# Performance work log

Measured on AMD Instinct MI355X. Metric: run time of the kernel, lower is better.

Reference implementation:

```python
import jax, jax.numpy as jnp
import numpy as np

N_NODES = 1_000_000   # nodal points, 3 DOFs each
N_ELEMS = 500_000     # H8 (8-node hexahedral) elements
N_TYPES = 64          # distinct element stiffness matrices (24x24)


def setup_inputs() -> dict:
    key = jax.random.key(0)
    k1, k2, k3, k4 = jax.random.split(key, 4)
    U = jax.random.normal(k1, (N_NODES, 3), dtype=jnp.float32)
    filters = jax.random.normal(k2, (N_TYPES, 24, 24), dtype=jnp.float32)
    H8types = jax.random.randint(k3, (N_ELEMS,), 0, N_TYPES, dtype=jnp.int32)
    nodIdx = jax.random.randint(k4, (N_ELEMS, 8), 0, N_NODES, dtype=jnp.int32)
    return {"U": U, "filters": filters, "H8types": H8types, "nodIdx": nodIdx}


def reference(U, filters, H8types, nodIdx):
    """FEM stiffness matvec KU = sum_e scatter(K_type(e) @ gather(U, e)).

    U:       [N, 3]      nodal displacements (3 DOFs per node)
    filters: [T, 24, 24] per-type element stiffness matrices
    H8types: [E]         element type index into filters
    nodIdx:  [E, 8]      element -> node connectivity
    returns KU: [N, 3]
    """
    E = nodIdx.shape[0]
    # gather the 8 nodes x 3 DOFs of each element -> [E, 24]
    ue = U[nodIdx].reshape(E, 24)
    # per-type stiffness for each element -> [E, 24, 24]
    Ke = filters[H8types]
    # per-element force vector f_e = K_e @ u_e -> [E, 24]
    fe = jnp.einsum('eij,ej->ei', Ke, ue)
    # scatter-add element forces back to nodal DOFs
    KU = jnp.zeros_like(U).at[nodIdx.reshape(-1)].add(fe.reshape(E * 8, 3))
    return KU
```

## Files before the change

kernel.cpp:

```cpp
#include <hip/hip_runtime.h>


#define NTYPES    64
#define KSTRIDE   580
#define RSHIFT    11
#define RNODES    2048
#define MAXB      512
#define CAP       10240
#define K1_TPB    1024
#define K1_EPT    2
#define K1_CHUNK  (K1_TPB * K1_EPT)
#define K2_TPB    1024
#define PREP_TPB  256

typedef int          nint4  __attribute__((ext_vector_type(4)));
typedef unsigned int nuint2 __attribute__((ext_vector_type(2)));
typedef unsigned int nuint4 __attribute__((ext_vector_type(4)));

__device__ __forceinline__ unsigned bf16_rne(float f) {
    unsigned b = __float_as_uint(f);
    return (b + 0x7FFFu + ((b >> 16) & 1u)) >> 16;
}


__global__ __launch_bounds__(PREP_TPB) void pack_u_kernel(
    const float* __restrict__ U, nuint2* __restrict__ Ub,
    float* __restrict__ KU, unsigned* __restrict__ tails,
    int n_nodes, int n_buckets)
{
    int n = blockIdx.x * PREP_TPB + threadIdx.x;
    if (n < n_buckets) tails[n] = 0;
    if (n >= n_nodes) return;
    const float* up = U + (size_t)n * 3;
    unsigned bx = bf16_rne(up[0]);
    unsigned by = bf16_rne(up[1]);
    unsigned bz = bf16_rne(up[2]);
    nuint2 v = { bx | (by << 16), bz };
    Ub[n] = v;
    KU[3 * n + 0] = 0.f;
    KU[3 * n + 1] = 0.f;
    KU[3 * n + 2] = 0.f;
}


__global__ __launch_bounds__(K1_TPB, 4) void feconv_bin_kernel(
    const nuint2* __restrict__ Ub,
    const float* __restrict__ K,
    const int*   __restrict__ types,
    const int*   __restrict__ nodIdx,
    float*       __restrict__ KU,
    unsigned*    __restrict__ tails,
    nuint2*      __restrict__ recs,
    int n_elems, int n_buckets)
{
    extern __shared__ float sK[];
    __shared__ unsigned       sCnt[MAXB];
    __shared__ unsigned       sBase[MAXB];
    __shared__ unsigned       sTCnt[NTYPES];
    __shared__ unsigned       sTOff[NTYPES];
    __shared__ unsigned short sOrder[K1_CHUNK];
    __shared__ unsigned char  sType[K1_CHUNK];

    for (int w = threadIdx.x; w < NTYPES * 576; w += K1_TPB) {
        int t = w / 576;
        int r = w - t * 576;
        sK[t * KSTRIDE + r] = K[w];
    }
    for (int i = threadIdx.x; i < n_buckets; i += K1_TPB) sCnt[i] = 0;
    if (threadIdx.x < NTYPES) sTCnt[threadIdx.x] = 0;
    __syncthreads();

    const int base = blockIdx.x * K1_CHUNK;
    int cnt_chunk = n_elems - base;
    if (cnt_chunk > K1_CHUNK) cnt_chunk = K1_CHUNK;

    int myT[K1_EPT];
#pragma unroll
    for (int k = 0; k < K1_EPT; ++k) {
        int li = threadIdx.x + k * K1_TPB;
        myT[k] = -1;
        if (li < cnt_chunk) {
            int t = __builtin_nontemporal_load(&types[base + li]);
            myT[k] = t;
            sType[li] = (unsigned char)t;
            atomicAdd(&sTCnt[t], 1u);
        }
    }
    __syncthreads();

    if (threadIdx.x < NTYPES) {
        unsigned v = sTCnt[threadIdx.x];
        unsigned s = v;
#pragma unroll
        for (int d = 1; d < NTYPES; d <<= 1) {
            unsigned o = __shfl_up(s, d, 64);
            if ((int)threadIdx.x >= d) s += o;
        }
        sTOff[threadIdx.x] = s - v;
        sTCnt[threadIdx.x] = 0;
    }
    __syncthreads();

#pragma unroll
    for (int k = 0; k < K1_EPT; ++k) {
        int li = threadIdx.x + k * K1_TPB;
        if (myT[k] >= 0) {
            unsigned p = sTOff[myT[k]] + atomicAdd(&sTCnt[myT[k]], 1u);
            sOrder[p] = (unsigned short)li;
        }
    }
    __syncthreads();

    int     nodes[K1_EPT][8];
    int     tt[K1_EPT];
    nuint2  uu[K1_EPT][8];

#pragma unroll
    for (int k = 0; k < K1_EPT; ++k) {
        int slot = threadIdx.x + k * K1_TPB;
        tt[k] = -1;
        if (slot < cnt_chunk) {
            int li = sOrder[slot];
            int e  = base + li;
            tt[k] = sType[li];
            const nint4* q = (const nint4*)(nodIdx + (size_t)e * 8);
            nint4 a = q[0];
            nint4 b = q[1];
            nodes[k][0] = a.x; nodes[k][1] = a.y; nodes[k][2] = a.z; nodes[k][3] = a.w;
            nodes[k][4] = b.x; nodes[k][5] = b.y; nodes[k][6] = b.z; nodes[k][7] = b.w;
#pragma unroll
            for (int j = 0; j < 8; ++j)
                uu[k][j] = Ub[nodes[k][j]];
#pragma unroll
            for (int j = 0; j < 8; ++j)
                atomicAdd(&sCnt[(unsigned)nodes[k][j] >> RSHIFT], 1u);
        }
    }
    __syncthreads();

    for (int b = threadIdx.x; b < n_buckets; b += K1_TPB) {
        unsigned c = sCnt[b];
        sBase[b] = c ? atomicAdd(&tails[b], c) : 0u;
        sCnt[b] = 0;
    }
    __syncthreads();

#pragma unroll
    for (int k = 0; k < K1_EPT; ++k) {
        if (tt[k] < 0) continue;

        float ue[24];
#pragma unroll
        for (int j = 0; j < 8; ++j) {
            nuint2 v = uu[k][j];
            ue[3 * j + 0] = __uint_as_float(v.x << 16);
            ue[3 * j + 1] = __uint_as_float(v.x & 0xFFFF0000u);
            ue[3 * j + 2] = __uint_as_float(v.y << 16);
        }

        const float4* Kt4 = (const float4*)(sK + tt[k] * KSTRIDE);
#pragma unroll
        for (int j = 0; j < 8; ++j) {
            float a0 = 0.f, a1 = 0.f, a2 = 0.f;
#pragma unroll
            for (int q = 0; q < 6; ++q) {
                float4 k0 = Kt4[(3 * j + 0) * 6 + q];
                float4 k1 = Kt4[(3 * j + 1) * 6 + q];
                float4 k2 = Kt4[(3 * j + 2) * 6 + q];
                float u0 = ue[4 * q + 0], u1 = ue[4 * q + 1];
                float u2 = ue[4 * q + 2], u3 = ue[4 * q + 3];
                a0 += k0.x * u0 + k0.y * u1 + k0.z * u2 + k0.w * u3;
                a1 += k1.x * u0 + k1.y * u1 + k1.z * u2 + k1.w * u3;
                a2 += k2.x * u0 + k2.y * u1 + k2.z * u2 + k2.w * u3;
            }
            unsigned n = (unsigned)nodes[k][j];
            unsigned b = n >> RSHIFT;
            unsigned pos = sBase[b] + atomicAdd(&sCnt[b], 1u);
            if (pos < CAP) {
                unsigned local = n & (RNODES - 1);
                nuint2 r = { bf16_rne(a0) | (bf16_rne(a1) << 16),
                             bf16_rne(a2) | (local << 16) };
                recs[(size_t)b * CAP + pos] = r;
            } else {
                atomicAdd(&KU[(size_t)n * 3 + 0], a0);
                atomicAdd(&KU[(size_t)n * 3 + 1], a1);
                atomicAdd(&KU[(size_t)n * 3 + 2], a2);
            }
        }
    }
}


__global__ __launch_bounds__(K2_TPB) void feconv_acc_kernel(
    const nuint2*   __restrict__ recs,
    const unsigned* __restrict__ tails,
    float*          __restrict__ KU,
    int n_nodes)
{
    __shared__ float sAcc[RNODES * 3];
    const int b = blockIdx.x;

    for (int i = threadIdx.x; i < RNODES * 3; i += K2_TPB) sAcc[i] = 0.f;
    __syncthreads();

    unsigned cnt = tails[b];
    if (cnt > CAP) cnt = CAP;
    const nuint2* base = recs + (size_t)b * CAP;
    const nuint4* base4 = (const nuint4*)base;

    unsigned npairs = cnt >> 1;
    for (unsigned i = threadIdx.x; i < npairs; i += K2_TPB) {
        nuint4 p = base4[i];
        unsigned o0 = (p.y >> 16) * 3;
        atomicAdd(&sAcc[o0 + 0], __uint_as_float(p.x << 16));
        atomicAdd(&sAcc[o0 + 1], __uint_as_float(p.x & 0xFFFF0000u));
        atomicAdd(&sAcc[o0 + 2], __uint_as_float(p.y << 16));
        unsigned o1 = (p.w >> 16) * 3;
        atomicAdd(&sAcc[o1 + 0], __uint_as_float(p.z << 16));
        atomicAdd(&sAcc[o1 + 1], __uint_as_float(p.z & 0xFFFF0000u));
        atomicAdd(&sAcc[o1 + 2], __uint_as_float(p.w << 16));
    }
    if ((cnt & 1u) && threadIdx.x == 0) {
        nuint2 r = base[cnt - 1];
        unsigned o = (r.y >> 16) * 3;
        atomicAdd(&sAcc[o + 0], __uint_as_float(r.x << 16));
        atomicAdd(&sAcc[o + 1], __uint_as_float(r.x & 0xFFFF0000u));
        atomicAdd(&sAcc[o + 2], __uint_as_float(r.y << 16));
    }
    __syncthreads();

    const int nbase = b * RNODES;
    int limit = n_nodes - nbase;
    if (limit > RNODES) limit = RNODES;
    limit *= 3;
    float* out = KU + (size_t)nbase * 3;
    for (int i = threadIdx.x; i < limit; i += K2_TPB) out[i] += sAcc[i];
}


__global__ __launch_bounds__(256) void feconv_elem_kernel(
    const float* __restrict__ U, const float* __restrict__ K,
    const int* __restrict__ types, const int* __restrict__ nodIdx,
    float* __restrict__ KU, int n_elems)
{
    int e = blockIdx.x * blockDim.x + threadIdx.x;
    if (e >= n_elems) return;
    int t = types[e];
    const int4* idx4 = (const int4*)(nodIdx + (size_t)e * 8);
    int4 iA = idx4[0], iB = idx4[1];
    int nodes[8] = {iA.x, iA.y, iA.z, iA.w, iB.x, iB.y, iB.z, iB.w};
    float ue[24];
#pragma unroll
    for (int j = 0; j < 8; ++j) {
        const float* up = U + (size_t)nodes[j] * 3;
        ue[3 * j + 0] = up[0]; ue[3 * j + 1] = up[1]; ue[3 * j + 2] = up[2];
    }
    const float* Kt = K + (size_t)t * 576;
#pragma unroll
    for (int i = 0; i < 24; ++i) {
        const float4* row = (const float4*)(Kt + i * 24);
        float acc = 0.f;
#pragma unroll
        for (int q = 0; q < 6; ++q) {
            float4 k = row[q];
            acc += k.x * ue[4 * q + 0] + k.y * ue[4 * q + 1]
                 + k.z * ue[4 * q + 2] + k.w * ue[4 * q + 3];
        }
        atomicAdd(&KU[(size_t)nodes[i / 3] * 3 + (i % 3)], acc);
    }
}

extern "C" void kernel_launch(void* const* d_in, const int* in_sizes, int n_in,
                              void* d_out, int out_size, void* d_ws, size_t ws_size,
                              hipStream_t stream) {
    const float* U      = (const float*)d_in[0];
    const float* Kf     = (const float*)d_in[1];
    const int*   types  = (const int*)d_in[2];
    const int*   nodIdx = (const int*)d_in[3];
    float*       KU     = (float*)d_out;

    const int n_elems = in_sizes[2];
    const int n_nodes = in_sizes[0] / 3;
    const int n_buckets = (n_nodes + RNODES - 1) / RNODES;

    const size_t ub_off  = 4096;
    const size_t rec_off = ub_off + (((size_t)n_nodes * 8 + 255) & ~255ull);
    const size_t need    = rec_off + (size_t)n_buckets * CAP * 8;

    if (n_buckets <= MAXB && ws_size >= need) {
        unsigned* tails = (unsigned*)d_ws;
        nuint2*   Ub    = (nuint2*)((char*)d_ws + ub_off);
        nuint2*   recs  = (nuint2*)((char*)d_ws + rec_off);

        int gridP = (n_nodes + PREP_TPB - 1) / PREP_TPB;
        pack_u_kernel<<<gridP, PREP_TPB, 0, stream>>>(
            U, Ub, KU, tails, n_nodes, n_buckets);

        size_t lds_bytes = (size_t)NTYPES * KSTRIDE * sizeof(float);
        int grid1 = (n_elems + K1_CHUNK - 1) / K1_CHUNK;
        feconv_bin_kernel<<<grid1, K1_TPB, lds_bytes, stream>>>(
            Ub, Kf, types, nodIdx, KU, tails, recs, n_elems, n_buckets);
        feconv_acc_kernel<<<n_buckets, K2_TPB, 0, stream>>>(
            recs, tails, KU, n_nodes);
    } else {
        (void)hipMemsetAsync(KU, 0, (size_t)out_size * sizeof(float), stream);
        int block = 256;
        int grid = (n_elems + block - 1) / block;
        feconv_elem_kernel<<<grid, block, 0, stream>>>(
            U, Kf, types, nodIdx, KU, n_elems);
    }
}
```

Before: 214.2 us.

## Read stiffness matrices from global memory instead of staging in LDS

Removes the per-block copy of all 64 stiffness matrices (about 148 KB) into shared memory, so the binning kernel reads K directly from global memory through the caches. Because elements are sorted by type within each block, neighbouring threads tend to read the same K rows. The block shrinks to 512 threads with one element per thread and higher occupancy hints, which also removes the per-block staging cost. In exchange, every multiply-accumulate now loads K from the L1/L2 caches instead of LDS, and each block has fewer elements to amortise its binning overhead.

Result: slower. 256.5 us (+19.8%).

```diff
diff --git a/kernel.cpp b/kernel.cpp
--- a/kernel.cpp
+++ b/kernel.cpp
@@ -2,13 +2,12 @@
 
 
 #define NTYPES    64
-#define KSTRIDE   580
 #define RSHIFT    11
 #define RNODES    2048
 #define MAXB      512
 #define CAP       10240
-#define K1_TPB    1024
-#define K1_EPT    2
+#define K1_TPB    512
+#define K1_EPT    1
 #define K1_CHUNK  (K1_TPB * K1_EPT)
 #define K2_TPB    1024
 #define PREP_TPB  256
@@ -43,7 +42,7 @@
 }
 
 
-__global__ __launch_bounds__(K1_TPB, 4) void feconv_bin_kernel(
+__global__ __launch_bounds__(K1_TPB, 6) void feconv_bin_kernel(
     const nuint2* __restrict__ Ub,
     const float* __restrict__ K,
     const int*   __restrict__ types,
@@ -53,7 +52,6 @@
     nuint2*      __restrict__ recs,
     int n_elems, int n_buckets)
 {
-    extern __shared__ float sK[];
     __shared__ unsigned       sCnt[MAXB];
     __shared__ unsigned       sBase[MAXB];
     __shared__ unsigned       sTCnt[NTYPES];
@@ -61,11 +59,6 @@
     __shared__ unsigned short sOrder[K1_CHUNK];
     __shared__ unsigned char  sType[K1_CHUNK];
 
-    for (int w = threadIdx.x; w < NTYPES * 576; w += K1_TPB) {
-        int t = w / 576;
-        int r = w - t * 576;
-        sK[t * KSTRIDE + r] = K[w];
-    }
     for (int i = threadIdx.x; i < n_buckets; i += K1_TPB) sCnt[i] = 0;
     if (threadIdx.x < NTYPES) sTCnt[threadIdx.x] = 0;
     __syncthreads();
@@ -74,14 +67,12 @@
     int cnt_chunk = n_elems - base;
     if (cnt_chunk > K1_CHUNK) cnt_chunk = K1_CHUNK;
 
-    int myT[K1_EPT];
-#pragma unroll
-    for (int k = 0; k < K1_EPT; ++k) {
-        int li = threadIdx.x + k * K1_TPB;
-        myT[k] = -1;
+    int myT = -1;
+    {
+        int li = threadIdx.x;
         if (li < cnt_chunk) {
             int t = __builtin_nontemporal_load(&types[base + li]);
-            myT[k] = t;
+            myT = t;
             sType[li] = (unsigned char)t;
             atomicAdd(&sTCnt[t], 1u);
         }
@@ -101,40 +92,31 @@
     }
     __syncthreads();
 
-#pragma unroll
-    for (int k = 0; k < K1_EPT; ++k) {
-        int li = threadIdx.x + k * K1_TPB;
-        if (myT[k] >= 0) {
-            unsigned p = sTOff[myT[k]] + atomicAdd(&sTCnt[myT[k]], 1u);
-            sOrder[p] = (unsigned short)li;
-        }
-    }
-    __syncthreads();
-
-    int     nodes[K1_EPT][8];
-    int     tt[K1_EPT];
-    nuint2  uu[K1_EPT][8];
-
-#pragma unroll
-    for (int k = 0; k < K1_EPT; ++k) {
-        int slot = threadIdx.x + k * K1_TPB;
-        tt[k] = -1;
-        if (slot < cnt_chunk) {
-            int li = sOrder[slot];
-            int e  = base + li;
-            tt[k] = sType[li];
-            const nint4* q = (const nint4*)(nodIdx + (size_t)e * 8);
-            nint4 a = q[0];
-            nint4 b = q[1];
-            nodes[k][0] = a.x; nodes[k][1] = a.y; nodes[k][2] = a.z; nodes[k][3] = a.w;
-            nodes[k][4] = b.x; nodes[k][5] = b.y; nodes[k][6] = b.z; nodes[k][7] = b.w;
-#pragma unroll
-            for (int j = 0; j < 8; ++j)
-                uu[k][j] = Ub[nodes[k][j]];
-#pragma unroll
-            for (int j = 0; j < 8; ++j)
-                atomicAdd(&sCnt[(unsigned)nodes[k][j] >> RSHIFT], 1u);
-        }
+    if (myT >= 0) {
+        unsigned p = sTOff[myT] + atomicAdd(&sTCnt[myT], 1u);
+        sOrder[p] = (unsigned short)threadIdx.x;
+    }
+    __syncthreads();
+
+    int    tt = -1;
+    int    nodes[8];
+    nuint2 uu[8];
+
+    if (threadIdx.x < cnt_chunk) {
+        int li = sOrder[threadIdx.x];
+        int e  = base + li;
+        tt = sType[li];
+        const nint4* q = (const nint4*)(nodIdx + (size_t)e * 8);
+        nint4 a = q[0];
+        nint4 b = q[1];
+        nodes[0] = a.x; nodes[1] = a.y; nodes[2] = a.z; nodes[3] = a.w;
+        nodes[4] = b.x; nodes[5] = b.y; nodes[6] = b.z; nodes[7] = b.w;
+#pragma unroll
+        for (int j = 0; j < 8; ++j)
+            uu[j] = Ub[nodes[j]];
+#pragma unroll
+        for (int j = 0; j < 8; ++j)
+            atomicAdd(&sCnt[(unsigned)nodes[j] >> RSHIFT], 1u);
     }
     __syncthreads();
 
@@ -145,20 +127,17 @@
     }
     __syncthreads();
 
-#pragma unroll
-    for (int k = 0; k < K1_EPT; ++k) {
-        if (tt[k] < 0) continue;
-
+    if (tt >= 0) {
         float ue[24];
 #pragma unroll
         for (int j = 0; j < 8; ++j) {
-            nuint2 v = uu[k][j];
+            nuint2 v = uu[j];
             ue[3 * j + 0] = __uint_as_float(v.x << 16);
             ue[3 * j + 1] = __uint_as_float(v.x & 0xFFFF0000u);
             ue[3 * j + 2] = __uint_as_float(v.y << 16);
         }
 
-        const float4* Kt4 = (const float4*)(sK + tt[k] * KSTRIDE);
+        const float4* Kt4 = (const float4*)(K + (size_t)tt * 576);
 #pragma unroll
         for (int j = 0; j < 8; ++j) {
             float a0 = 0.f, a1 = 0.f, a2 = 0.f;
@@ -173,7 +152,7 @@
                 a1 += k1.x * u0 + k1.y * u1 + k1.z * u2 + k1.w * u3;
                 a2 += k2.x * u0 + k2.y * u1 + k2.z * u2 + k2.w * u3;
             }
-            unsigned n = (unsigned)nodes[k][j];
+            unsigned n = (unsigned)nodes[j];
             unsigned b = n >> RSHIFT;
             unsigned pos = sBase[b] + atomicAdd(&sCnt[b], 1u);
             if (pos < CAP) {
@@ -296,9 +275,8 @@
         pack_u_kernel<<<gridP, PREP_TPB, 0, stream>>>(
             U, Ub, KU, tails, n_nodes, n_buckets);
 
-        size_t lds_bytes = (size_t)NTYPES * KSTRIDE * sizeof(float);
         int grid1 = (n_elems + K1_CHUNK - 1) / K1_CHUNK;
-        feconv_bin_kernel<<<grid1, K1_TPB, lds_bytes, stream>>>(
+        feconv_bin_kernel<<<grid1, K1_TPB, 0, stream>>>(
             Ub, Kf, types, nodIdx, KU, tails, recs, n_elems, n_buckets);
         feconv_acc_kernel<<<n_buckets, K2_TPB, 0, stream>>>(
             recs, tails, KU, n_nodes);
```

## Split element type range across block pairs to halve LDS stiffness footprint

Applied to the files above, without the earlier changes.

Each element window is now handled by two blocks, each loading only half of the stiffness-matrix types into LDS and processing the elements whose type falls in its half. This halves per-block LDS so more blocks can reside per CU (launch bounds raised), at the cost of doubling the K preload and the type reads per window, and leaving half-empty thread slots. Bucket granularity is also coarsened (larger node ranges, larger capacity), and KSTRIDE padding is removed, which may introduce LDS bank conflicts.

Result: slower. 274.3 us (+28.1%).

```diff
diff --git a/kernel.cpp b/kernel.cpp
--- a/kernel.cpp
+++ b/kernel.cpp
@@ -2,14 +2,14 @@
 
 
 #define NTYPES    64
-#define KSTRIDE   580
-#define RSHIFT    11
-#define RNODES    2048
-#define MAXB      512
-#define CAP       10240
+#define HTYPES    32
+#define KWORDS    576
+#define RSHIFT    12
+#define RNODES    4096
+#define MAXB      256
+#define CAP       20480
 #define K1_TPB    1024
-#define K1_EPT    2
-#define K1_CHUNK  (K1_TPB * K1_EPT)
+#define WCHUNK    2048
 #define K2_TPB    1024
 #define PREP_TPB  256
 
@@ -43,7 +43,7 @@
 }
 
 
-__global__ __launch_bounds__(K1_TPB, 4) void feconv_bin_kernel(
+__global__ __launch_bounds__(K1_TPB, 8) void feconv_bin_kernel(
     const nuint2* __restrict__ Ub,
     const float* __restrict__ K,
     const int*   __restrict__ types,
@@ -56,44 +56,43 @@
     extern __shared__ float sK[];
     __shared__ unsigned       sCnt[MAXB];
     __shared__ unsigned       sBase[MAXB];
-    __shared__ unsigned       sTCnt[NTYPES];
-    __shared__ unsigned       sTOff[NTYPES];
-    __shared__ unsigned short sOrder[K1_CHUNK];
-    __shared__ unsigned char  sType[K1_CHUNK];
-
-    for (int w = threadIdx.x; w < NTYPES * 576; w += K1_TPB) {
-        int t = w / 576;
-        int r = w - t * 576;
-        sK[t * KSTRIDE + r] = K[w];
-    }
+    __shared__ unsigned       sTCnt[HTYPES];
+    __shared__ unsigned       sTOff[HTYPES];
+    __shared__ unsigned short sOrder[WCHUNK];
+
+    const int window = blockIdx.x >> 1;
+    const int typeLo = (blockIdx.x & 1) * HTYPES;
+    const int base   = window * WCHUNK;
+    int cnt_chunk = n_elems - base;
+    if (cnt_chunk > WCHUNK) cnt_chunk = WCHUNK;
+
+    for (int w = threadIdx.x; w < HTYPES * KWORDS; w += K1_TPB)
+        sK[w] = K[(size_t)typeLo * KWORDS + w];
     for (int i = threadIdx.x; i < n_buckets; i += K1_TPB) sCnt[i] = 0;
-    if (threadIdx.x < NTYPES) sTCnt[threadIdx.x] = 0;
-    __syncthreads();
-
-    const int base = blockIdx.x * K1_CHUNK;
-    int cnt_chunk = n_elems - base;
-    if (cnt_chunk > K1_CHUNK) cnt_chunk = K1_CHUNK;
-
-    int myT[K1_EPT];
-#pragma unroll
-    for (int k = 0; k < K1_EPT; ++k) {
+    if (threadIdx.x < HTYPES) sTCnt[threadIdx.x] = 0;
+    __syncthreads();
+
+    int myT[2];
+#pragma unroll
+    for (int k = 0; k < 2; ++k) {
         int li = threadIdx.x + k * K1_TPB;
         myT[k] = -1;
         if (li < cnt_chunk) {
-            int t = __builtin_nontemporal_load(&types[base + li]);
-            myT[k] = t;
-            sType[li] = (unsigned char)t;
-            atomicAdd(&sTCnt[t], 1u);
-        }
-    }
-    __syncthreads();
-
-    if (threadIdx.x < NTYPES) {
+            int rel = __builtin_nontemporal_load(&types[base + li]) - typeLo;
+            if ((unsigned)rel < HTYPES) {
+                myT[k] = rel;
+                atomicAdd(&sTCnt[rel], 1u);
+            }
+        }
+    }
+    __syncthreads();
+
+    if (threadIdx.x < HTYPES) {
         unsigned v = sTCnt[threadIdx.x];
         unsigned s = v;
 #pragma unroll
-        for (int d = 1; d < NTYPES; d <<= 1) {
-            unsigned o = __shfl_up(s, d, 64);
+        for (int d = 1; d < HTYPES; d <<= 1) {
+            unsigned o = __shfl_up(s, d, HTYPES);
             if ((int)threadIdx.x >= d) s += o;
         }
         sTOff[threadIdx.x] = s - v;
@@ -102,27 +101,30 @@
     __syncthreads();
 
 #pragma unroll
-    for (int k = 0; k < K1_EPT; ++k) {
-        int li = threadIdx.x + k * K1_TPB;
+    for (int k = 0; k < 2; ++k) {
         if (myT[k] >= 0) {
+            int li = threadIdx.x + k * K1_TPB;
             unsigned p = sTOff[myT[k]] + atomicAdd(&sTCnt[myT[k]], 1u);
-            sOrder[p] = (unsigned short)li;
-        }
-    }
-    __syncthreads();
-
-    int     nodes[K1_EPT][8];
-    int     tt[K1_EPT];
-    nuint2  uu[K1_EPT][8];
-
-#pragma unroll
-    for (int k = 0; k < K1_EPT; ++k) {
+            sOrder[p] = (unsigned short)(li | (myT[k] << 11));
+        }
+    }
+    __syncthreads();
+
+    const int cntHalf = (int)(sTOff[HTYPES - 1] + sTCnt[HTYPES - 1]);
+
+    int    tt[2];
+    int    nodes[2][8];
+    nuint2 uu[2][8];
+
+#pragma unroll
+    for (int k = 0; k < 2; ++k) {
         int slot = threadIdx.x + k * K1_TPB;
         tt[k] = -1;
-        if (slot < cnt_chunk) {
-            int li = sOrder[slot];
-            int e  = base + li;
-            tt[k] = sType[li];
+        if (slot < cntHalf) {
+            unsigned od = sOrder[slot];
+            int li  = od & (WCHUNK - 1);
+            tt[k]   = od >> 11;
+            int e   = base + li;
             const nint4* q = (const nint4*)(nodIdx + (size_t)e * 8);
             nint4 a = q[0];
             nint4 b = q[1];
@@ -146,7 +148,7 @@
     __syncthreads();
 
 #pragma unroll
-    for (int k = 0; k < K1_EPT; ++k) {
+    for (int k = 0; k < 2; ++k) {
         if (tt[k] < 0) continue;
 
         float ue[24];
@@ -158,7 +160,7 @@
             ue[3 * j + 2] = __uint_as_float(v.y << 16);
         }
 
-        const float4* Kt4 = (const float4*)(sK + tt[k] * KSTRIDE);
+        const float4* Kt4 = (const float4*)(sK + (size_t)tt[k] * KWORDS);
 #pragma unroll
         for (int j = 0; j < 8; ++j) {
             float a0 = 0.f, a1 = 0.f, a2 = 0.f;
@@ -296,8 +298,9 @@
         pack_u_kernel<<<gridP, PREP_TPB, 0, stream>>>(
             U, Ub, KU, tails, n_nodes, n_buckets);
 
-        size_t lds_bytes = (size_t)NTYPES * KSTRIDE * sizeof(float);
-        int grid1 = (n_elems + K1_CHUNK - 1) / K1_CHUNK;
+        size_t lds_bytes = (size_t)HTYPES * KWORDS * sizeof(float);
+        int nWindows = (n_elems + WCHUNK - 1) / WCHUNK;
+        int grid1 = nWindows * 2;
         feconv_bin_kernel<<<grid1, K1_TPB, lds_bytes, stream>>>(
             Ub, Kf, types, nodIdx, KU, tails, recs, n_elems, n_buckets);
         feconv_acc_kernel<<<n_buckets, K2_TPB, 0, stream>>>(
```

## Store element stiffness matrices in LDS as fp16 and halve block size

Applied to the files above, without the earlier changes.

Converts the 64 stiffness matrices to half precision when loading them into shared memory, halving LDS footprint from ~148KB to ~75KB. Block size drops to 512 threads so that more blocks can be resident per CU. The element type is also packed into the sort-order short, which removes the sType array. This adds half-to-float conversions in the inner loop and loses precision on the K values.

Result: slower. 223.0 us (+4.1%).

```diff
diff --git a/kernel.cpp b/kernel.cpp
--- a/kernel.cpp
+++ b/kernel.cpp
@@ -1,13 +1,14 @@
 #include <hip/hip_runtime.h>
+#include <hip/hip_fp16.h>
 
 
 #define NTYPES    64
-#define KSTRIDE   580
+#define KHALF     584
 #define RSHIFT    11
 #define RNODES    2048
 #define MAXB      512
 #define CAP       10240
-#define K1_TPB    1024
+#define K1_TPB    512
 #define K1_EPT    2
 #define K1_CHUNK  (K1_TPB * K1_EPT)
 #define K2_TPB    1024
@@ -20,6 +21,11 @@
 __device__ __forceinline__ unsigned bf16_rne(float f) {
     unsigned b = __float_as_uint(f);
     return (b + 0x7FFFu + ((b >> 16) & 1u)) >> 16;
+}
+
+__device__ __forceinline__ float2 h2f(unsigned h) {
+    __half2 x = *reinterpret_cast<__half2*>(&h);
+    return __half22float2(x);
 }
 
 
@@ -53,18 +59,17 @@
     nuint2*      __restrict__ recs,
     int n_elems, int n_buckets)
 {
-    extern __shared__ float sK[];
+    extern __shared__ __half sKh[];
     __shared__ unsigned       sCnt[MAXB];
     __shared__ unsigned       sBase[MAXB];
     __shared__ unsigned       sTCnt[NTYPES];
     __shared__ unsigned       sTOff[NTYPES];
     __shared__ unsigned short sOrder[K1_CHUNK];
-    __shared__ unsigned char  sType[K1_CHUNK];
 
     for (int w = threadIdx.x; w < NTYPES * 576; w += K1_TPB) {
         int t = w / 576;
         int r = w - t * 576;
-        sK[t * KSTRIDE + r] = K[w];
+        sKh[t * KHALF + r] = __float2half(K[w]);
     }
     for (int i = threadIdx.x; i < n_buckets; i += K1_TPB) sCnt[i] = 0;
     if (threadIdx.x < NTYPES) sTCnt[threadIdx.x] = 0;
@@ -82,7 +87,6 @@
         if (li < cnt_chunk) {
             int t = __builtin_nontemporal_load(&types[base + li]);
             myT[k] = t;
-            sType[li] = (unsigned char)t;
             atomicAdd(&sTCnt[t], 1u);
         }
     }
@@ -103,26 +107,27 @@
 
 #pragma unroll
     for (int k = 0; k < K1_EPT; ++k) {
-        int li = threadIdx.x + k * K1_TPB;
         if (myT[k] >= 0) {
+            int li = threadIdx.x + k * K1_TPB;
             unsigned p = sTOff[myT[k]] + atomicAdd(&sTCnt[myT[k]], 1u);
-            sOrder[p] = (unsigned short)li;
-        }
-    }
-    __syncthreads();
-
-    int     nodes[K1_EPT][8];
-    int     tt[K1_EPT];
-    nuint2  uu[K1_EPT][8];
+            sOrder[p] = (unsigned short)(li | (myT[k] << 10));
+        }
+    }
+    __syncthreads();
+
+    int    tt[K1_EPT];
+    int    nodes[K1_EPT][8];
+    nuint2 uu[K1_EPT][8];
 
 #pragma unroll
     for (int k = 0; k < K1_EPT; ++k) {
         int slot = threadIdx.x + k * K1_TPB;
         tt[k] = -1;
         if (slot < cnt_chunk) {
-            int li = sOrder[slot];
-            int e  = base + li;
-            tt[k] = sType[li];
+            unsigned od = sOrder[slot];
+            int li  = od & (K1_CHUNK - 1);
+            tt[k]   = od >> 10;
+            int e   = base + li;
             const nint4* q = (const nint4*)(nodIdx + (size_t)e * 8);
             nint4 a = q[0];
             nint4 b = q[1];
@@ -158,20 +163,23 @@
             ue[3 * j + 2] = __uint_as_float(v.y << 16);
         }
 
-        const float4* Kt4 = (const float4*)(sK + tt[k] * KSTRIDE);
+        const nuint2* KtQ = (const nuint2*)(sKh + (size_t)tt[k] * KHALF);
 #pragma unroll
         for (int j = 0; j < 8; ++j) {
             float a0 = 0.f, a1 = 0.f, a2 = 0.f;
 #pragma unroll
             for (int q = 0; q < 6; ++q) {
-                float4 k0 = Kt4[(3 * j + 0) * 6 + q];
-                float4 k1 = Kt4[(3 * j + 1) * 6 + q];
-                float4 k2 = Kt4[(3 * j + 2) * 6 + q];
+                nuint2 k0 = KtQ[(3 * j + 0) * 6 + q];
+                nuint2 k1 = KtQ[(3 * j + 1) * 6 + q];
+                nuint2 k2 = KtQ[(3 * j + 2) * 6 + q];
                 float u0 = ue[4 * q + 0], u1 = ue[4 * q + 1];
                 float u2 = ue[4 * q + 2], u3 = ue[4 * q + 3];
-                a0 += k0.x * u0 + k0.y * u1 + k0.z * u2 + k0.w * u3;
-                a1 += k1.x * u0 + k1.y * u1 + k1.z * u2 + k1.w * u3;
-                a2 += k2.x * u0 + k2.y * u1 + k2.z * u2 + k2.w * u3;
+                float2 f0a = h2f(k0.x), f0b = h2f(k0.y);
+                float2 f1a = h2f(k1.x), f1b = h2f(k1.y);
+                float2 f2a = h2f(k2.x), f2b = h2f(k2.y);
+                a0 += f0a.x * u0 + f0a.y * u1 + f0b.x * u2 + f0b.y * u3;
+                a1 += f1a.x * u0 + f1a.y * u1 + f1b.x * u2 + f1b.y * u3;
+                a2 += f2a.x * u0 + f2a.y * u1 + f2b.x * u2 + f2b.y * u3;
             }
             unsigned n = (unsigned)nodes[k][j];
             unsigned b = n >> RSHIFT;
@@ -296,7 +304,7 @@
         pack_u_kernel<<<gridP, PREP_TPB, 0, stream>>>(
             U, Ub, KU, tails, n_nodes, n_buckets);
 
-        size_t lds_bytes = (size_t)NTYPES * KSTRIDE * sizeof(float);
+        size_t lds_bytes = (size_t)NTYPES * KHALF * sizeof(__half);
         int grid1 = (n_elems + K1_CHUNK - 1) / K1_CHUNK;
         feconv_bin_kernel<<<grid1, K1_TPB, lds_bytes, stream>>>(
             Ub, Kf, types, nodIdx, KU, tails, recs, n_elems, n_buckets);
```
